# Kernel tuning notes

Hardware: AMD Instinct MI355X
Metric: run time of the kernel (lower is better)

The kernel has to match this reference:

```python
import jax, jax.numpy as jnp
import numpy as np

# dims
B, C, N, T = 8, 64, 500, 12      # batch, channels (c_in=c_out=nhid), nodes, time
H, F = 4, 64                      # nheads, nhid per head
GDEP = 2
ALPHA = 0.05                      # mixprop residual mix
LEAK = 0.2                        # leakyrelu slope in attention


def setup_inputs() -> dict:
    key = jax.random.key(0)
    ks = jax.random.split(key, 9)
    x = jax.random.normal(ks[0], (B, C, N, T), jnp.float32)
    adj = (jax.random.uniform(ks[1], (N, N)) < 0.05).astype(jnp.float32)
    # per-head GAT params stacked on head axis
    W = jax.random.normal(ks[2], (H, C, F), jnp.float32) * 0.05   # head projection
    a1 = jax.random.normal(ks[3], (H, F), jnp.float32) * 0.05     # a[:F]
    a2 = jax.random.normal(ks[4], (H, F), jnp.float32) * 0.05     # a[F:]
    # GAT output mlp: Conv2d 1x1, (H*F) -> F
    Wg = jax.random.normal(ks[5], (F, H * F), jnp.float32) * 0.05
    bg = jnp.zeros((F,), jnp.float32)
    # mixprop mlp: (GDEP+1)*C -> C
    Wm = jax.random.normal(ks[6], (C, (GDEP + 1) * C), jnp.float32) * 0.05
    bm = jnp.zeros((C,), jnp.float32)
    return {"x": x, "adj": adj, "W": W, "a1": a1, "a2": a2,
            "Wg": Wg, "bg": bg, "Wm": Wm, "bm": bm}


def _gat(h, mask, W, a1, a2, Wg, bg):
    # h: [B,C,N,T]; eval mode (dropout = identity)
    hp = jnp.transpose(h, (0, 3, 2, 1))                 # [B,T,N,C]
    Wh = jnp.einsum('btnc,hcf->bhtnf', hp, W)           # [B,H,T,N,F]
    e1 = jnp.einsum('bhtnf,hf->bhtn', Wh, a1)           # src term
    e2 = jnp.einsum('bhtnf,hf->bhtn', Wh, a2)           # dst term
    e = jax.nn.leaky_relu(e1[..., :, None] + e2[..., None, :], LEAK)  # [B,H,T,N,N]
    e = jnp.where(mask, e, jnp.float32(-9e15))
    att = jax.nn.softmax(e, axis=-1)
    hpr = jax.nn.elu(jnp.einsum('bhtnm,bhtmf->bhtnf', att, Wh))       # [B,H,T,N,F]
    # concat heads along channel dim -> [B, H*F, N, T]
    cat = jnp.transpose(hpr, (0, 1, 4, 3, 2)).reshape(B, H * F, N, T)
    # 1x1 conv mix
    return jnp.einsum('bcnt,oc->bont', cat, Wg) + bg[None, :, None, None]


def reference(x, adj, W, a1, a2, Wg, bg, Wm, bm):
    mask = (adj + jnp.eye(N, dtype=adj.dtype)) > 0      # self-loops added
    h = x
    outs = [h]
    for _ in range(GDEP):
        h = ALPHA * x + (1.0 - ALPHA) * _gat(h, mask, W, a1, a2, Wg, bg)
        outs.append(h)
    ho = jnp.concatenate(outs, axis=1)                  # [B,(GDEP+1)*C,N,T]
    return jnp.einsum('bcnt,oc->bont', ho, Wm) + bm[None, :, None, None]
```

## Files before the change

### kernel.cpp

```cpp
#include <hip/hip_runtime.h>
#include <hip/hip_bf16.h>
#include <math.h>

#define BB 8
#define CC 64
#define NN 500
#define TT 12
#define HH 4
#define FF 64
#define CT (CC*TT)
#define HF (HH*FF)
#define NBT (HH*TT)
#define NBHT (BB*NBT)
#define NROWS (BB*HH*TT*NN)
#define NNODE (BB*NN)
#define BSR 200
#define KST 68
#define WTS 520

typedef unsigned short ushort_t;
typedef unsigned int uint_t;
typedef __attribute__((ext_vector_type(8))) short short8;
typedef __attribute__((ext_vector_type(4))) float floatx4;

static __device__ __forceinline__ ushort_t f2bf(float v) {
    __hip_bfloat16 h = __float2bfloat16(v);
    ushort_t u;
    __builtin_memcpy(&u, &h, 2);
    return u;
}

static __device__ __forceinline__ uint_t pkbf(float a, float b) {
    __hip_bfloat162 h = __float22bfloat162_rn(make_float2(a, b));
    uint_t u;
    __builtin_memcpy(&u, &h, 4);
    return u;
}

__global__ __launch_bounds__(256) void k016_setup(const float* __restrict__ adj,
                                                  const float* __restrict__ W,
                                                  const float* __restrict__ a1,
                                                  const float* __restrict__ a2,
                                                  const float* __restrict__ Wm,
                                                  const float* __restrict__ Wg,
                                                  const float* __restrict__ x,
                                                  uint_t* __restrict__ maskbits,
                                                  float* __restrict__ p1,
                                                  float* __restrict__ p2,
                                                  ushort_t* __restrict__ WmB,
                                                  ushort_t* __restrict__ WgB,
                                                  ushort_t* __restrict__ WtB,
                                                  float* __restrict__ xT,
                                                  ushort_t* __restrict__ WhT) {
    __shared__ float tile[16*776];
    int blk = blockIdx.x;
    if (blk < 32) {
        int idx = blk * 256 + threadIdx.x;
        int n = idx >> 4, j = idx & 15;
        uint_t v = 0;
        if (n < NN) {
            int m0 = j * 32;
            for (int i = 0; i < 32; ++i) {
                int m = m0 + i;
                bool p = (m < NN) && (adj[n*NN + m] > 0.f || m == n);
                v |= (p ? 1u : 0u) << i;
            }
        }
        maskbits[idx] = v;
        return;
    }
    if (blk < 209) {
        int idx = (blk - 32) * 256 + threadIdx.x;
        if (idx < HH*CC) {
            int h = idx / CC, c = idx % CC;
            float s1 = 0.f, s2 = 0.f;
            for (int f = 0; f < FF; ++f) {
                float w = W[(h*CC + c)*FF + f];
                s1 += w * a1[h*FF + f];
                s2 += w * a2[h*FF + f];
            }
            p1[idx] = s1; p2[idx] = s2;
        }
        int j = idx - HH*CC;
        if (j >= 0 && j < CC*3*CC) {
            WmB[j] = f2bf(Wm[j]);
        }
        int j2 = idx - (HH*CC + CC*3*CC);
        if (j2 >= 0 && j2 < FF*HF) {
            WgB[j2] = f2bf(Wg[j2]);
        }
        int j3 = idx - (HH*CC + CC*3*CC + FF*HF);
        if (j3 >= 0 && j3 < HH*CC*FF) {
            int h = j3 >> 12, rem = j3 & 4095;
            int f = rem >> 6, c = rem & 63;
            WtB[j3] = f2bf(W[h*4096 + c*64 + f]);
        }
        return;
    }
    if (blk >= 465) {
        int row = (blk - 465) * 256 + threadIdx.x;
        uint_t* p = (uint_t*)(WhT + (size_t)row * 512 + 500);
        #pragma unroll
        for (int j = 0; j < 6; ++j) p[j] = 0;
        return;
    }
    int xblk = blk - 209;
    int b  = xblk >> 5;
    int n0 = (xblk & 31) * 16;
    for (int idx = threadIdx.x; idx < CC*16*TT; idx += 256) {
        int c   = idx / (16*TT);
        int rem = idx % (16*TT);
        int nl  = rem / TT;
        int t   = rem % TT;
        int n   = n0 + nl;
        if (n < NN)
            tile[nl*776 + c*TT + t] = x[((b*CC + c)*NN + n)*TT + t];
    }
    __syncthreads();
    for (int idx = threadIdx.x; idx < 16*CT; idx += 256) {
        int nl = idx / CT;
        int j  = idx % CT;
        int n  = n0 + nl;
        if (n < NN)
            xT[(size_t)(b*NN + n)*CT + j] = tile[nl*776 + j];
    }
}

__global__ __launch_bounds__(256) void k2_wh_e(const float* __restrict__ hin,
                                               const ushort_t* __restrict__ WtB,
                                               const float* __restrict__ p1,
                                               const float* __restrict__ p2,
                                               ushort_t* __restrict__ WhT,
                                               float* __restrict__ e1,
                                               float* __restrict__ e2) {
    __shared__ char uni[4*TT*WTS*2];
    __shared__ ushort_t Bs[8][TT*KST];
    float (*hL)[CT] = (float(*)[CT])uni;
    int tid  = threadIdx.x;
    int wid  = tid >> 6;
    int lane = tid & 63;
    int quad = lane >> 4;
    int r    = lane & 15;
    int b    = blockIdx.x / 63;
    int nl0  = (blockIdx.x % 63) * 8;

    for (int i = tid; i < 8*(CT/4); i += 256) {
        int u = i / (CT/4), j = i % (CT/4);
        int node = b*NN + nl0 + u;
        if (node > NNODE-1) node = NNODE-1;
        ((float4*)hL[u])[j] = ((const float4*)(hin + (size_t)node*CT))[j];
    }
    __syncthreads();
    for (int e = tid; e < 8*CT; e += 256) {
        int u = e / CT, i = e % CT;
        int c = i / TT, t = i % TT;
        Bs[u][t*KST + c] = f2bf(hL[u][i]);
    }
    {
        int t2 = lane & 15, h2 = lane >> 4;
        if (t2 < TT) {
            for (int pass = 0; pass < 2; ++pass) {
                int u  = wid + pass*4;
                int nl = nl0 + u;
                if (nl < NN) {
                    const float* hLw = hL[u];
                    float s1 = 0.f, s2 = 0.f;
                    for (int c = 0; c < CC; ++c) {
                        float v = hLw[c*TT + t2];
                        s1 += v * p1[h2*CC + c];
                        s2 += v * p2[h2*CC + c];
                    }
                    int idx = ((b*HH + h2)*TT + t2)*NN + nl;
                    e1[idx] = s1;
                    e2[idx] = s2;
                }
            }
        }
    }
    __syncthreads();

    ushort_t* WTl = (ushort_t*)uni + wid*(TT*WTS);

    short8 Afr[4][2];
    #pragma unroll
    for (int mt = 0; mt < 4; ++mt)
        #pragma unroll
        for (int kc = 0; kc < 2; ++kc)
            Afr[mt][kc] = *(const short8*)(WtB + wid*4096 +
                                           (mt*16 + r)*64 + kc*32 + quad*8);

    int rcl = r < TT ? r : TT-1;

    for (int u = 0; u < 8; ++u) {
        bool valid = (nl0 + u) < NN;
        floatx4 C[4];
        #pragma unroll
        for (int mt = 0; mt < 4; ++mt) C[mt] = (floatx4){0.f,0.f,0.f,0.f};
        #pragma unroll
        for (int kc = 0; kc < 2; ++kc) {
            short8 bfr = *(const short8*)&Bs[u][rcl*KST + kc*32 + quad*8];
            #pragma unroll
            for (int mt = 0; mt < 4; ++mt)
                C[mt] = __builtin_amdgcn_mfma_f32_16x16x32_bf16(Afr[mt][kc], bfr, C[mt], 0, 0, 0);
        }
        if (r < TT) {
            #pragma unroll
            for (int mt = 0; mt < 4; ++mt) {
                #pragma unroll
                for (int reg = 0; reg < 4; ++reg) {
                    int f = mt*16 + quad*4 + reg;
                    WTl[r*WTS + f*8 + u] = valid ? f2bf(C[mt][reg]) : (ushort_t)0;
                }
            }
        }
    }

    {
        size_t base = ((size_t)(b*NBT + wid*TT) * 64) * 512 + nl0;
        #pragma unroll
        for (int t = 0; t < TT; ++t) {
            short8 v = *(const short8*)&WTl[t*WTS + lane*8];
            *(short8*)(WhT + base + ((size_t)t*64 + lane)*512) = v;
        }
    }
}

__global__ __launch_bounds__(256, 3) void k3_attn(const ushort_t* __restrict__ WhT,
                                                  const float* __restrict__ e1,
                                                  const float* __restrict__ e2,
                                                  const uint_t* __restrict__ maskbits,
                                                  ushort_t* __restrict__ hprB) {
    __shared__ float  e2s[512];
    __shared__ uint_t mks[256*17];
    int tid  = threadIdx.x;
    int wid  = tid >> 6;
    int lane = tid & 63;
    int bht  = blockIdx.x >> 1;
    int half = blockIdx.x & 1;
    int b    = bht / NBT;
    int ht   = bht % NBT;

    const float* e1p = e1 + (size_t)bht * NN;
    const float* e2p = e2 + (size_t)bht * NN;
    const ushort_t* WT = WhT + (size_t)bht * 64 * 512;
    const float L2E = 1.4426950408889634f;

    {
        int i = tid;
        e2s[i] = (i < NN) ? e2p[i] * L2E : 0.f;
        i = tid + 256;
        e2s[i] = (i < NN) ? e2p[i] * L2E : 0.f;
    }
    for (int i = tid; i < 256*16; i += 256) {
        int rl = i >> 4, dw = i & 15;
        mks[rl*17 + dw] = maskbits[(half*256 + rl)*16 + dw];
    }
    __syncthreads();

    int quad = lane >> 4;
    int r    = lane & 15;

    const short8 ONES = {0x3F80,0x3F80,0x3F80,0x3F80,
                         0x3F80,0x3F80,0x3F80,0x3F80};

    float e1v[4];
    #pragma unroll
    for (int u = 0; u < 4; ++u) {
        int nrow = half*256 + (wid*4 + u)*16 + r;
        e1v[u] = ((nrow < NN) ? e1p[nrow] : 0.f) * L2E;
    }
    int rl0 = wid*64 + r;

    const ushort_t* WTr = WT + (size_t)r * 512;

    floatx4 C[4][4];
    floatx4 Cs[4];
    #pragma unroll
    for (int u = 0; u < 4; ++u) {
        Cs[u] = (floatx4){0.f,0.f,0.f,0.f};
        #pragma unroll
        for (int ft = 0; ft < 4; ++ft) C[u][ft] = (floatx4){0.f,0.f,0.f,0.f};
    }

    #pragma unroll
    for (int ki = 0; ki < 16; ++ki) {
        int kb = ki*32 + quad*8;

        short8 b0 = *(const short8*)(WTr + 0*8192 + kb);
        short8 b1 = *(const short8*)(WTr + 1*8192 + kb);
        short8 b2 = *(const short8*)(WTr + 2*8192 + kb);
        short8 b3 = *(const short8*)(WTr + 3*8192 + kb);

        float4 ea = *(const float4*)&e2s[kb];
        float4 eb = *(const float4*)&e2s[kb + 4];
        float ev[8] = {ea.x,ea.y,ea.z,ea.w, eb.x,eb.y,eb.z,eb.w};

        #pragma unroll
        for (int u = 0; u < 4; ++u) {
            uint_t md    = mks[(rl0 + u*16)*17 + ki];
            uint_t mbits = md >> (quad*8);
            union { uint_t w[4]; short8 s; } av;
            #pragma unroll
            for (int p = 0; p < 4; ++p) {
                float s0 = e1v[u] + ev[2*p];
                float s1 = e1v[u] + ev[2*p+1];
                float g0 = fmaxf(s0, 0.2f*s0);
                float g1 = fmaxf(s1, 0.2f*s1);
                float x0 = __builtin_amdgcn_exp2f(g0);
                float x1 = __builtin_amdgcn_exp2f(g1);
                x0 = (mbits & (1u << (2*p)))     ? x0 : 0.f;
                x1 = (mbits & (1u << (2*p + 1))) ? x1 : 0.f;
                av.w[p] = pkbf(x0, x1);
            }
            C[u][0] = __builtin_amdgcn_mfma_f32_16x16x32_bf16(av.s, b0, C[u][0], 0, 0, 0);
            C[u][1] = __builtin_amdgcn_mfma_f32_16x16x32_bf16(av.s, b1, C[u][1], 0, 0, 0);
            C[u][2] = __builtin_amdgcn_mfma_f32_16x16x32_bf16(av.s, b2, C[u][2], 0, 0, 0);
            C[u][3] = __builtin_amdgcn_mfma_f32_16x16x32_bf16(av.s, b3, C[u][3], 0, 0, 0);
            Cs[u]   = __builtin_amdgcn_mfma_f32_16x16x32_bf16(av.s, ONES, Cs[u], 0, 0, 0);
        }
    }

    #pragma unroll
    for (int u = 0; u < 4; ++u) {
        int n0 = half*256 + (wid*4 + u)*16;
        #pragma unroll
        for (int reg = 0; reg < 4; ++reg) {
            int n = n0 + quad*4 + reg;
            if (n < NN) {
                float inv = 1.0f / Cs[u][reg];
                size_t base = ((size_t)(b*NN + n)*NBT + ht)*FF;
                #pragma unroll
                for (int ft = 0; ft < 4; ++ft) {
                    float v = C[u][ft][reg] * inv;
                    v = v > 0.f ? v : __expf(v) - 1.f;
                    hprB[base + ft*16 + r] = f2bf(v);
                }
            }
        }
    }
}

__global__ __launch_bounds__(256) void k4_mfma(const ushort_t* __restrict__ hprB,
                                               const ushort_t* __restrict__ WgB,
                                               const float* __restrict__ bg,
                                               const float* __restrict__ xT,
                                               float* __restrict__ hnext) {
    __shared__ float S[4][CT];
    int wid  = threadIdx.x >> 6;
    int lane = threadIdx.x & 63;
    int quad = lane >> 4;
    int r    = lane & 15;

    short8 Afr[4][8];
    #pragma unroll
    for (int ot = 0; ot < 4; ++ot)
        #pragma unroll
        for (int kc = 0; kc < 8; ++kc)
            Afr[ot][kc] = *(const short8*)(WgB + (size_t)(ot*16 + r)*HF + kc*32 + quad*8);

    float4 bgv[4];
    #pragma unroll
    for (int ot = 0; ot < 4; ++ot)
        bgv[ot] = *(const float4*)(bg + ot*16 + quad*4);

    int tcl = r < TT ? r : TT-1;

    int node = blockIdx.x*4 + wid;
    const ushort_t* P = hprB + (size_t)node * (NBT*FF);

    floatx4 C[4];
    #pragma unroll
    for (int ot = 0; ot < 4; ++ot) C[ot] = (floatx4){0.f,0.f,0.f,0.f};

    #pragma unroll
    for (int kc = 0; kc < 8; ++kc) {
        int k = kc*32 + quad*8;
        int h = k >> 6, f0 = k & 63;
        short8 bfr = *(const short8*)(P + (h*TT + tcl)*FF + f0);
        #pragma unroll
        for (int ot = 0; ot < 4; ++ot)
            C[ot] = __builtin_amdgcn_mfma_f32_16x16x32_bf16(Afr[ot][kc], bfr, C[ot], 0, 0, 0);
    }

    if (r < TT) {
        #pragma unroll
        for (int ot = 0; ot < 4; ++ot) {
            #pragma unroll
            for (int reg = 0; reg < 4; ++reg) {
                int o = ot*16 + quad*4 + reg;
                S[wid][o*TT + r] = C[ot][reg] + bgv[ot][reg];
            }
        }
    }
    {
        const float4* xp4 = (const float4*)(xT + (size_t)node * CT);
        float4* ho4 = (float4*)(hnext + (size_t)node * CT);
        const float4* S4 = (const float4*)S[wid];
        #pragma unroll
        for (int j = 0; j < 3; ++j) {
            int i = lane + j*64;
            float4 xv = xp4[i];
            float4 sv = S4[i];
            float4 ov;
            ov.x = 0.05f*xv.x + 0.95f*sv.x;
            ov.y = 0.05f*xv.y + 0.95f*sv.y;
            ov.z = 0.05f*xv.z + 0.95f*sv.z;
            ov.w = 0.05f*xv.w + 0.95f*sv.w;
            ho4[i] = ov;
        }
    }
}

__global__ __launch_bounds__(256) void k45_fused(const ushort_t* __restrict__ hprB,
                                                 const ushort_t* __restrict__ WgB,
                                                 const float* __restrict__ bg,
                                                 const float* __restrict__ xT,
                                                 const float* __restrict__ h1,
                                                 const ushort_t* __restrict__ WmB,
                                                 const float* __restrict__ bm,
                                                 float* __restrict__ out) {
    __shared__ ushort_t Bs[4][TT*BSR];
    __shared__ float    So[4][CT];
    int wid  = threadIdx.x >> 6;
    int lane = threadIdx.x & 63;
    int quad = lane >> 4;
    int r    = lane & 15;

    int node = blockIdx.x*4 + wid;
    ushort_t* Bw = Bs[wid];

    {
        const float* xp = xT + (size_t)node*CT + lane*TT;
        const float* hp = h1 + (size_t)node*CT + lane*TT;
        float4 x0 = *(const float4*)(xp);
        float4 x1 = *(const float4*)(xp + 4);
        float4 x2 = *(const float4*)(xp + 8);
        float4 g0 = *(const float4*)(hp);
        float4 g1 = *(const float4*)(hp + 4);
        float4 g2 = *(const float4*)(hp + 8);
        float xa[12] = {x0.x,x0.y,x0.z,x0.w, x1.x,x1.y,x1.z,x1.w,
                        x2.x,x2.y,x2.z,x2.w};
        float ha[12] = {g0.x,g0.y,g0.z,g0.w, g1.x,g1.y,g1.z,g1.w,
                        g2.x,g2.y,g2.z,g2.w};
        #pragma unroll
        for (int t = 0; t < TT; ++t) {
            Bw[t*BSR + lane]      = f2bf(xa[t]);
            Bw[t*BSR + 64 + lane] = f2bf(ha[t]);
        }
    }

    {
        short8 Afr[4][8];
        #pragma unroll
        for (int ot = 0; ot < 4; ++ot)
            #pragma unroll
            for (int kc = 0; kc < 8; ++kc)
                Afr[ot][kc] = *(const short8*)(WgB + (size_t)(ot*16 + r)*HF + kc*32 + quad*8);
        float4 bgv[4];
        #pragma unroll
        for (int ot = 0; ot < 4; ++ot)
            bgv[ot] = *(const float4*)(bg + ot*16 + quad*4);

        int tcl = r < TT ? r : TT-1;
        const ushort_t* P = hprB + (size_t)node * (NBT*FF);

        floatx4 C[4];
        #pragma unroll
        for (int ot = 0; ot < 4; ++ot) C[ot] = (floatx4){0.f,0.f,0.f,0.f};
        #pragma unroll
        for (int kc = 0; kc < 8; ++kc) {
            int k = kc*32 + quad*8;
            int h = k >> 6, f0 = k & 63;
            short8 bfr = *(const short8*)(P + (h*TT + tcl)*FF + f0);
            #pragma unroll
            for (int ot = 0; ot < 4; ++ot)
                C[ot] = __builtin_amdgcn_mfma_f32_16x16x32_bf16(Afr[ot][kc], bfr, C[ot], 0, 0, 0);
        }

        if (r < TT) {
            const float* xp = xT + (size_t)node * CT;
            #pragma unroll
            for (int ot = 0; ot < 4; ++ot) {
                #pragma unroll
                for (int rp = 0; rp < 4; rp += 2) {
                    int o = ot*16 + quad*4 + rp;
                    float v0 = C[ot][rp]   + bgv[ot][rp];
                    float v1 = C[ot][rp+1] + bgv[ot][rp+1];
                    float h20 = 0.05f*xp[o*TT + r]       + 0.95f*v0;
                    float h21 = 0.05f*xp[(o+1)*TT + r]   + 0.95f*v1;
                    *(uint_t*)&Bw[r*BSR + 128 + o] = pkbf(h20, h21);
                }
            }
        }
    }

    {
        short8 Am[4][6];
        #pragma unroll
        for (int ot = 0; ot < 4; ++ot)
            #pragma unroll
            for (int kc = 0; kc < 6; ++kc)
                Am[ot][kc] = *(const short8*)(WmB + (size_t)(ot*16 + r)*(3*CC) + kc*32 + quad*8);

        int trd = r < TT ? r : TT-1;
        floatx4 C2[4];
        #pragma unroll
        for (int ot = 0; ot < 4; ++ot) C2[ot] = (floatx4){0.f,0.f,0.f,0.f};
        #pragma unroll
        for (int kc = 0; kc < 6; ++kc) {
            short8 bfr = *(const short8*)&Bw[trd*BSR + kc*32 + quad*8];
            #pragma unroll
            for (int ot = 0; ot < 4; ++ot)
                C2[ot] = __builtin_amdgcn_mfma_f32_16x16x32_bf16(Am[ot][kc], bfr, C2[ot], 0, 0, 0);
        }

        if (r < TT) {
            #pragma unroll
            for (int ot = 0; ot < 4; ++ot) {
                float4 bmv = *(const float4*)(bm + ot*16 + quad*4);
                #pragma unroll
                for (int reg = 0; reg < 4; ++reg) {
                    int o = ot*16 + quad*4 + reg;
                    So[wid][o*TT + r] = C2[ot][reg] + bmv[reg];
                }
            }
        }
    }
    __syncthreads();

    {
        int o = threadIdx.x >> 2;
        int q = threadIdx.x & 3;
        int nodeq = blockIdx.x*4 + q;
        int bq = nodeq / NN, nq = nodeq % NN;
        float* op = out + ((size_t)(bq*CC + o)*NN + nq)*TT;
        const float* Sp = So[q] + o*TT;
        *(float4*)&op[0] = *(const float4*)&Sp[0];
        *(float4*)&op[4] = *(const float4*)&Sp[4];
        *(float4*)&op[8] = *(const float4*)&Sp[8];
    }
}

extern "C" void kernel_launch(void* const* d_in, const int* in_sizes, int n_in,
                              void* d_out, int out_size, void* d_ws, size_t ws_size,
                              hipStream_t stream) {
    const float* x   = (const float*)d_in[0];
    const float* adj = (const float*)d_in[1];
    const float* W   = (const float*)d_in[2];
    const float* a1  = (const float*)d_in[3];
    const float* a2  = (const float*)d_in[4];
    const float* Wg  = (const float*)d_in[5];
    const float* bg  = (const float*)d_in[6];
    const float* Wm  = (const float*)d_in[7];
    const float* bm  = (const float*)d_in[8];
    float* out = (float*)d_out;

    char* ws = (char*)d_ws;
    size_t off = 0;
    auto alloc = [&](size_t bytes) -> void* {
        void* p = ws + off;
        off += (bytes + 255) & ~(size_t)255;
        return p;
    };

    uint_t* maskbits = (uint_t*)alloc((size_t)512 * 16 * 4);
    float* p1   = (float*)alloc(HH*CC * sizeof(float));
    float* p2   = (float*)alloc(HH*CC * sizeof(float));
    ushort_t* WmB = (ushort_t*)alloc((size_t)CC*3*CC * 2);
    ushort_t* WgB = (ushort_t*)alloc((size_t)FF*HF * 2);
    ushort_t* WtB = (ushort_t*)alloc((size_t)HH*CC*FF * 2);
    float* xT   = (float*)alloc((size_t)NNODE * CT * sizeof(float));
    ushort_t* WhT  = (ushort_t*)alloc((size_t)NBHT * 64 * 512 * 2);
    ushort_t* hprB = (ushort_t*)alloc((size_t)NNODE * NBT * FF * 2);
    float* e1   = (float*)alloc((size_t)NROWS * sizeof(float));
    float* e2   = (float*)alloc((size_t)NROWS * sizeof(float));
    float* h1   = (float*)alloc((size_t)NNODE * CT * sizeof(float));
    (void)ws_size;

    k016_setup<<<561, 256, 0, stream>>>(adj, W, a1, a2, Wm, Wg, x,
                                        maskbits, p1, p2, WmB, WgB, WtB, xT, WhT);

    k2_wh_e <<<8*63,    256, 0, stream>>>(xT, WtB, p1, p2, WhT, e1, e2);
    k3_attn <<<NBHT*2,  256, 0, stream>>>(WhT, e1, e2, maskbits, hprB);
    k4_mfma <<<NNODE/4, 256, 0, stream>>>(hprB, WgB, bg, xT, h1);

    k2_wh_e <<<8*63,    256, 0, stream>>>(h1, WtB, p1, p2, WhT, e1, e2);
    k3_attn <<<NBHT*2,  256, 0, stream>>>(WhT, e1, e2, maskbits, hprB);

    k45_fused<<<NNODE/4, 256, 0, stream>>>(hprB, WgB, bg, xT, h1, WmB, bm, out);
}
```

Baseline: 303.2 us.

## Store x and intermediate h1 as bf16 in t-major layout across kernels

Intermediate activations xT and h1 are now stored in bf16 with a [node][t][c] layout instead of fp32 [node][c][t]. k2 can copy them straight into its MFMA B-tile in shared memory without an fp32 staging buffer, and it drops a transpose/convert pass and a __syncthreads. k4 and k45 read and write the narrower format with vector loads. This halves the intermediate traffic and removes conversion work. In exchange, the residual x term and the e1/e2 logits are now computed from bf16-rounded values, which costs some accuracy.

```diff
diff --git a/kernel.cpp b/kernel.cpp
--- a/kernel.cpp
+++ b/kernel.cpp
@@ -30,6 +30,10 @@
     return u;
 }
 
+static __device__ __forceinline__ float bf2f(ushort_t u) {
+    return __uint_as_float(((uint_t)u) << 16);
+}
+
 static __device__ __forceinline__ uint_t pkbf(float a, float b) {
     __hip_bfloat162 h = __float22bfloat162_rn(make_float2(a, b));
     uint_t u;
@@ -50,7 +54,7 @@
                                                   ushort_t* __restrict__ WmB,
                                                   ushort_t* __restrict__ WgB,
                                                   ushort_t* __restrict__ WtB,
-                                                  float* __restrict__ xT,
+                                                  ushort_t* __restrict__ xB,
                                                   ushort_t* __restrict__ WhT) {
     __shared__ float tile[16*776];
     int blk = blockIdx.x;
@@ -117,25 +121,27 @@
             tile[nl*776 + c*TT + t] = x[((b*CC + c)*NN + n)*TT + t];
     }
     __syncthreads();
-    for (int idx = threadIdx.x; idx < 16*CT; idx += 256) {
-        int nl = idx / CT;
-        int j  = idx % CT;
-        int n  = n0 + nl;
-        if (n < NN)
-            xT[(size_t)(b*NN + n)*CT + j] = tile[nl*776 + j];
-    }
-}
-
-__global__ __launch_bounds__(256) void k2_wh_e(const float* __restrict__ hin,
+    for (int idx = threadIdx.x; idx < 16*384; idx += 256) {
+        int nl = idx / 384, j = idx % 384;
+        int t = j >> 5, c2 = j & 31;
+        int n = n0 + nl;
+        if (n < NN) {
+            float v0 = tile[nl*776 + (2*c2)*TT + t];
+            float v1 = tile[nl*776 + (2*c2 + 1)*TT + t];
+            *(uint_t*)&xB[(size_t)(b*NN + n)*CT + t*64 + 2*c2] = pkbf(v0, v1);
+        }
+    }
+}
+
+__global__ __launch_bounds__(256) void k2_wh_e(const ushort_t* __restrict__ hinB,
                                                const ushort_t* __restrict__ WtB,
                                                const float* __restrict__ p1,
                                                const float* __restrict__ p2,
                                                ushort_t* __restrict__ WhT,
                                                float* __restrict__ e1,
                                                float* __restrict__ e2) {
-    __shared__ char uni[4*TT*WTS*2];
+    __shared__ ushort_t WTu[4*TT*WTS];
     __shared__ ushort_t Bs[8][TT*KST];
-    float (*hL)[CT] = (float(*)[CT])uni;
     int tid  = threadIdx.x;
     int wid  = tid >> 6;
     int lane = tid & 63;
@@ -144,18 +150,16 @@
     int b    = blockIdx.x / 63;
     int nl0  = (blockIdx.x % 63) * 8;
 
-    for (int i = tid; i < 8*(CT/4); i += 256) {
-        int u = i / (CT/4), j = i % (CT/4);
+    for (int i = tid; i < 8*TT*8; i += 256) {
+        int u = i / 96, rem = i % 96;
+        int t = rem >> 3, c8 = rem & 7;
         int node = b*NN + nl0 + u;
         if (node > NNODE-1) node = NNODE-1;
-        ((float4*)hL[u])[j] = ((const float4*)(hin + (size_t)node*CT))[j];
+        short8 v = *(const short8*)(hinB + (size_t)node*CT + t*64 + c8*8);
+        *(short8*)&Bs[u][t*KST + c8*8] = v;
     }
     __syncthreads();
-    for (int e = tid; e < 8*CT; e += 256) {
-        int u = e / CT, i = e % CT;
-        int c = i / TT, t = i % TT;
-        Bs[u][t*KST + c] = f2bf(hL[u][i]);
-    }
+
     {
         int t2 = lane & 15, h2 = lane >> 4;
         if (t2 < TT) {
@@ -163,10 +167,10 @@
                 int u  = wid + pass*4;
                 int nl = nl0 + u;
                 if (nl < NN) {
-                    const float* hLw = hL[u];
+                    const ushort_t* Bu = Bs[u];
                     float s1 = 0.f, s2 = 0.f;
                     for (int c = 0; c < CC; ++c) {
-                        float v = hLw[c*TT + t2];
+                        float v = bf2f(Bu[t2*KST + c]);
                         s1 += v * p1[h2*CC + c];
                         s2 += v * p2[h2*CC + c];
                     }
@@ -177,9 +181,8 @@
             }
         }
     }
-    __syncthreads();
-
-    ushort_t* WTl = (ushort_t*)uni + wid*(TT*WTS);
+
+    ushort_t* WTl = WTu + wid*(TT*WTS);
 
     short8 Afr[4][2];
     #pragma unroll
@@ -343,8 +346,8 @@
 __global__ __launch_bounds__(256) void k4_mfma(const ushort_t* __restrict__ hprB,
                                                const ushort_t* __restrict__ WgB,
                                                const float* __restrict__ bg,
-                                               const float* __restrict__ xT,
-                                               float* __restrict__ hnext) {
+                                               const ushort_t* __restrict__ xB,
+                                               ushort_t* __restrict__ h1B) {
     __shared__ float S[4][CT];
     int wid  = threadIdx.x >> 6;
     int lane = threadIdx.x & 63;
@@ -393,20 +396,23 @@
         }
     }
     {
-        const float4* xp4 = (const float4*)(xT + (size_t)node * CT);
-        float4* ho4 = (float4*)(hnext + (size_t)node * CT);
-        const float4* S4 = (const float4*)S[wid];
-        #pragma unroll
-        for (int j = 0; j < 3; ++j) {
-            int i = lane + j*64;
-            float4 xv = xp4[i];
-            float4 sv = S4[i];
-            float4 ov;
-            ov.x = 0.05f*xv.x + 0.95f*sv.x;
-            ov.y = 0.05f*xv.y + 0.95f*sv.y;
-            ov.z = 0.05f*xv.z + 0.95f*sv.z;
-            ov.w = 0.05f*xv.w + 0.95f*sv.w;
-            ho4[i] = ov;
+        const ushort_t* xp = xB + (size_t)node*CT;
+        ushort_t* hp = h1B + (size_t)node*CT;
+        const float* Sw = S[wid];
+        for (int task = lane; task < 96; task += 64) {
+            int t = task >> 3, c8 = task & 7;
+            short8 xv = *(const short8*)(xp + t*64 + c8*8);
+            union { uint_t w[4]; short8 s; } ov;
+            #pragma unroll
+            for (int p = 0; p < 4; ++p) {
+                int c0 = c8*8 + 2*p;
+                float x0 = bf2f((ushort_t)xv[2*p]);
+                float x1 = bf2f((ushort_t)xv[2*p+1]);
+                float v0 = 0.05f*x0 + 0.95f*Sw[c0*TT + t];
+                float v1 = 0.05f*x1 + 0.95f*Sw[(c0+1)*TT + t];
+                ov.w[p] = pkbf(v0, v1);
+            }
+            *(short8*)(hp + t*64 + c8*8) = ov.s;
         }
     }
 }
@@ -414,8 +420,8 @@
 __global__ __launch_bounds__(256) void k45_fused(const ushort_t* __restrict__ hprB,
                                                  const ushort_t* __restrict__ WgB,
                                                  const float* __restrict__ bg,
-                                                 const float* __restrict__ xT,
-                                                 const float* __restrict__ h1,
+                                                 const ushort_t* __restrict__ xB,
+                                                 const ushort_t* __restrict__ h1B,
                                                  const ushort_t* __restrict__ WmB,
                                                  const float* __restrict__ bm,
                                                  float* __restrict__ out) {
@@ -430,22 +436,12 @@
     ushort_t* Bw = Bs[wid];
 
     {
-        const float* xp = xT + (size_t)node*CT + lane*TT;
-        const float* hp = h1 + (size_t)node*CT + lane*TT;
-        float4 x0 = *(const float4*)(xp);
-        float4 x1 = *(const float4*)(xp + 4);
-        float4 x2 = *(const float4*)(xp + 8);
-        float4 g0 = *(const float4*)(hp);
-        float4 g1 = *(const float4*)(hp + 4);
-        float4 g2 = *(const float4*)(hp + 8);
-        float xa[12] = {x0.x,x0.y,x0.z,x0.w, x1.x,x1.y,x1.z,x1.w,
-                        x2.x,x2.y,x2.z,x2.w};
-        float ha[12] = {g0.x,g0.y,g0.z,g0.w, g1.x,g1.y,g1.z,g1.w,
-                        g2.x,g2.y,g2.z,g2.w};
-        #pragma unroll
-        for (int t = 0; t < TT; ++t) {
-            Bw[t*BSR + lane]      = f2bf(xa[t]);
-            Bw[t*BSR + 64 + lane] = f2bf(ha[t]);
+        const ushort_t* xp = xB  + (size_t)node*CT;
+        const ushort_t* hp = h1B + (size_t)node*CT;
+        for (int task = lane; task < 96; task += 64) {
+            int t = task >> 3, c8 = task & 7;
+            *(short8*)&Bw[t*BSR + c8*8]      = *(const short8*)(xp + t*64 + c8*8);
+            *(short8*)&Bw[t*BSR + 64 + c8*8] = *(const short8*)(hp + t*64 + c8*8);
         }
     }
 
@@ -478,7 +474,6 @@
         }
 
         if (r < TT) {
-            const float* xp = xT + (size_t)node * CT;
             #pragma unroll
             for (int ot = 0; ot < 4; ++ot) {
                 #pragma unroll
@@ -486,8 +481,10 @@
                     int o = ot*16 + quad*4 + rp;
                     float v0 = C[ot][rp]   + bgv[ot][rp];
                     float v1 = C[ot][rp+1] + bgv[ot][rp+1];
-                    float h20 = 0.05f*xp[o*TT + r]       + 0.95f*v0;
-                    float h21 = 0.05f*xp[(o+1)*TT + r]   + 0.95f*v1;
+                    float x0 = bf2f(Bw[r*BSR + o]);
+                    float x1 = bf2f(Bw[r*BSR + o + 1]);
+                    float h20 = 0.05f*x0 + 0.95f*v0;
+                    float h21 = 0.05f*x1 + 0.95f*v1;
                     *(uint_t*)&Bw[r*BSR + 128 + o] = pkbf(h20, h21);
                 }
             }
@@ -569,23 +566,23 @@
     ushort_t* WmB = (ushort_t*)alloc((size_t)CC*3*CC * 2);
     ushort_t* WgB = (ushort_t*)alloc((size_t)FF*HF * 2);
     ushort_t* WtB = (ushort_t*)alloc((size_t)HH*CC*FF * 2);
-    float* xT   = (float*)alloc((size_t)NNODE * CT * sizeof(float));
+    ushort_t* xB  = (ushort_t*)alloc((size_t)NNODE * CT * 2);
     ushort_t* WhT  = (ushort_t*)alloc((size_t)NBHT * 64 * 512 * 2);
     ushort_t* hprB = (ushort_t*)alloc((size_t)NNODE * NBT * FF * 2);
     float* e1   = (float*)alloc((size_t)NROWS * sizeof(float));
     float* e2   = (float*)alloc((size_t)NROWS * sizeof(float));
-    float* h1   = (float*)alloc((size_t)NNODE * CT * sizeof(float));
+    ushort_t* h1B = (ushort_t*)alloc((size_t)NNODE * CT * 2);
     (void)ws_size;
 
     k016_setup<<<561, 256, 0, stream>>>(adj, W, a1, a2, Wm, Wg, x,
-                                        maskbits, p1, p2, WmB, WgB, WtB, xT, WhT);
-
-    k2_wh_e <<<8*63,    256, 0, stream>>>(xT, WtB, p1, p2, WhT, e1, e2);
+                                        maskbits, p1, p2, WmB, WgB, WtB, xB, WhT);
+
+    k2_wh_e <<<8*63,    256, 0, stream>>>(xB, WtB, p1, p2, WhT, e1, e2);
     k3_attn <<<NBHT*2,  256, 0, stream>>>(WhT, e1, e2, maskbits, hprB);
-    k4_mfma <<<NNODE/4, 256, 0, stream>>>(hprB, WgB, bg, xT, h1);
-
-    k2_wh_e <<<8*63,    256, 0, stream>>>(h1, WtB, p1, p2, WhT, e1, e2);
+    k4_mfma <<<NNODE/4, 256, 0, stream>>>(hprB, WgB, bg, xB, h1B);
+
+    k2_wh_e <<<8*63,    256, 0, stream>>>(h1B, WtB, p1, p2, WhT, e1, e2);
     k3_attn <<<NBHT*2,  256, 0, stream>>>(WhT, e1, e2, maskbits, hprB);
 
-    k45_fused<<<NNODE/4, 256, 0, stream>>>(hprB, WgB, bg, xT, h1, WmB, bm, out);
-}
+    k45_fused<<<NNODE/4, 256, 0, stream>>>(hprB, WgB, bg, xB, h1B, WmB, bm, out);
+}
```

Result: no change. 298.7 us (-1.5%).
